# Performance work log

Measured on AMD Instinct MI355X. Metric: run time of the kernel, lower is better.

## Reference

```python
import math
import jax, jax.numpy as jnp
import numpy as np

V_NODES = 100000
E_EDGES = 800000
D_IN = 128
D_OUT = 128
H = 4
F_H = D_OUT // H
LEAK = 0.2


def _xavier(key, shape):
    fan_in, fan_out = shape[0], shape[1]
    lim = math.sqrt(6.0 / (fan_in + fan_out))
    return jax.random.uniform(key, shape, jnp.float32, -lim, lim)


def setup_inputs() -> dict:
    key = jax.random.key(0)
    ks = jax.random.split(key, 10)
    h = jax.random.normal(ks[0], (V_NODES, D_IN), jnp.float32)
    edge_index = jax.random.randint(ks[1], (2, E_EDGES), 0, V_NODES, jnp.int64)
    # omega in {+1, -1, 0}
    edge_weight = jax.random.randint(ks[2], (E_EDGES,), -1, 2).astype(jnp.float32)
    return {
        "h": h,
        "edge_index": edge_index,
        "edge_weight": edge_weight,
        "Wq": _xavier(ks[3], (D_IN, D_OUT)), "bq": jnp.zeros((D_OUT,), jnp.float32),
        "Wk": _xavier(ks[4], (D_IN, D_OUT)), "bk": jnp.zeros((D_OUT,), jnp.float32),
        "Wv": _xavier(ks[5], (D_IN, D_OUT)), "bv": jnp.zeros((D_OUT,), jnp.float32),
        "Wo": _xavier(ks[6], (D_OUT, D_OUT)), "bo": jnp.zeros((D_OUT,), jnp.float32),
        "We": _xavier(ks[7], (1, H)), "be": jnp.zeros((H,), jnp.float32),
        "gamma": jnp.ones((D_OUT,), jnp.float32), "beta": jnp.zeros((D_OUT,), jnp.float32),
    }


def _layer_norm(x, gamma, beta, eps=1e-5):
    mu = jnp.mean(x, axis=-1, keepdims=True)
    var = jnp.var(x, axis=-1, keepdims=True)
    return (x - mu) * jax.lax.rsqrt(var + eps) * gamma + beta


def reference(h, edge_index, edge_weight, Wq, bq, Wk, bk, Wv, bv, Wo, bo, We, be, gamma, beta):
    V = h.shape[0]
    Q = (h @ Wq + bq).reshape(V, H, F_H)
    K = (h @ Wk + bk).reshape(V, H, F_H)
    Vv = (h @ Wv + bv).reshape(V, H, F_H)

    src, tgt = edge_index[0], edge_index[1]
    # edge-aware bias: Proj(omega) with LeakyReLU, [E, H]
    edge_bias = jax.nn.leaky_relu(edge_weight[:, None] * We[0] + be, LEAK)

    # per-edge multi-head scores [E, H]
    attn_raw = jnp.einsum("ehf,ehf->eh", Q[src], K[tgt]) / math.sqrt(F_H)
    attn_raw = attn_raw + edge_bias  # ent_bias = 0 (add_entity_sim=False)
    attn_exp = jnp.exp(attn_raw)

    # degree-based softmax normalization over incoming edges of each target
    deg = jax.ops.segment_sum(attn_exp, tgt, num_segments=V) + 1e-16  # [V, H]
    attn_norm = attn_exp / deg[tgt]  # [E, H]  (dropout rate = 0)

    # weighted message aggregation: alpha * omega * (W_v h_src)
    msg = Vv[src] * attn_norm[:, :, None] * edge_weight[:, None, None]  # [E, H, F_H]
    out = jax.ops.segment_sum(msg, tgt, num_segments=V).reshape(V, H * F_H)

    out = out @ Wo + bo + h  # residual
    out = _layer_norm(out, gamma, beta)
    return jax.nn.leaky_relu(out, LEAK)
```

## Files before the change

kernel.cpp:

```cpp
#include <hip/hip_runtime.h>
#include <math.h>

#define V_NODES 100000
#define E_EDGES 800000
#define HEADS 4
#define FH 32
#define D 128
#define LEAK 0.2f
#define NB 8

__global__ __launch_bounds__(384) void qkv_kernel(
    const float* __restrict__ h,
    const float* __restrict__ Wq, const float* __restrict__ bq,
    const float* __restrict__ Wk, const float* __restrict__ bk,
    const float* __restrict__ Wv, const float* __restrict__ bv,
    float* __restrict__ Q, float* __restrict__ K, float* __restrict__ Vv)
{
    __shared__ float hsh[D][NB];
    const int tid  = threadIdx.x;
    const int base = blockIdx.x * NB;

    for (int idx = tid; idx < NB * D; idx += 384) {
        int n = idx >> 7, k = idx & 127;
        hsh[k][n] = h[(long)(base + n) * D + k];
    }
    __syncthreads();

    const int wsel = tid >> 7;
    const int col  = tid & 127;
    const float* W = (wsel == 0) ? Wq : (wsel == 1) ? Wk : Wv;
    const float* b = (wsel == 0) ? bq : (wsel == 1) ? bk : bv;
    float* O       = (wsel == 0) ? Q  : (wsel == 1) ? K  : Vv;

    float acc[NB];
#pragma unroll
    for (int n = 0; n < NB; n++) acc[n] = 0.f;

    for (int k = 0; k < D; k++) {
        float w = W[k * D + col];
#pragma unroll
        for (int n = 0; n < NB; n++) acc[n] += hsh[k][n] * w;
    }

    float bias = b[col];
#pragma unroll
    for (int n = 0; n < NB; n++) O[(long)(base + n) * D + col] = acc[n] + bias;
}

__global__ __launch_bounds__(256) void score_kernel(
    const int* __restrict__ src, const int* __restrict__ tgt,
    const float* __restrict__ ew,
    const float* __restrict__ Q, const float* __restrict__ K,
    const float* __restrict__ We, const float* __restrict__ be,
    float* __restrict__ attn_exp)
{
    int t = blockIdx.x * 256 + threadIdx.x;
    int e = t >> 4;
    int sub = t & 15;
    if (e >= E_EDGES) return;
    int s = src[e], tg = tgt[e];
    const float4* q4 = (const float4*)(Q + (long)s * D);
    const float4* k4 = (const float4*)(K + (long)tg * D);
    float4 a0 = q4[sub * 2], a1 = q4[sub * 2 + 1];
    float4 b0 = k4[sub * 2], b1 = k4[sub * 2 + 1];
    float p = a0.x * b0.x + a0.y * b0.y + a0.z * b0.z + a0.w * b0.w
            + a1.x * b1.x + a1.y * b1.y + a1.z * b1.z + a1.w * b1.w;
    p += __shfl_xor(p, 1);
    p += __shfl_xor(p, 2);
    if ((sub & 3) == 0) {
        int hh = sub >> 2;
        float w = ew[e];
        float bias = w * We[hh] + be[hh];
        bias = (bias > 0.f) ? bias : LEAK * bias;
        attn_exp[(long)e * 4 + hh] = __expf(p * 0.17677669529663687f + bias);
    }
}

__global__ __launch_bounds__(256) void hist_kernel(
    const int* __restrict__ tgt, int* __restrict__ rs)
{
    int e = blockIdx.x * 256 + threadIdx.x;
    if (e < E_EDGES) atomicAdd(&rs[tgt[e]], 1);
}

__global__ __launch_bounds__(1024) void scan_kernel(int* __restrict__ rs)
{
    __shared__ int part[1024];
    const int tid = threadIdx.x;
    const int CH = (V_NODES + 1023) / 1024;
    int begin = tid * CH;
    int end   = begin + CH; if (end > V_NODES) end = V_NODES;
    if (begin > V_NODES) begin = V_NODES;
    int s = 0;
    for (int i = begin; i < end; i++) s += rs[i];
    part[tid] = s;
    __syncthreads();
    for (int off = 1; off < 1024; off <<= 1) {
        int v = (tid >= off) ? part[tid - off] : 0;
        __syncthreads();
        part[tid] += v;
        __syncthreads();
    }
    int excl = (tid == 0) ? 0 : part[tid - 1];
    for (int i = begin; i < end; i++) {
        int c = rs[i];
        rs[i] = excl;
        excl += c;
    }
}

__global__ __launch_bounds__(256) void scatter_kernel(
    const int* __restrict__ tgt, int* __restrict__ rs, int* __restrict__ csr_e)
{
    int e = blockIdx.x * 256 + threadIdx.x;
    if (e >= E_EDGES) return;
    int pos = atomicAdd(&rs[tgt[e]], 1);
    csr_e[pos] = e;
}

__global__ __launch_bounds__(256) void agg_kernel(
    const int* __restrict__ rs, const int* __restrict__ csr_e,
    const int* __restrict__ src, const float* __restrict__ ew,
    const float* __restrict__ attn_exp,
    const float* __restrict__ Vv, float* __restrict__ out)
{
    int node = blockIdx.x * 4 + (threadIdx.x >> 6);
    if (node >= V_NODES) return;
    int lane = threadIdx.x & 63;
    int hh = lane >> 4;
    int j1 = rs[node];
    int j0 = node ? rs[node - 1] : 0;
    float acc0 = 0.f, acc1 = 0.f, deg = 0.f;
    for (int j = j0; j < j1; j++) {
        int e = csr_e[j];
        float4 att = *((const float4*)(attn_exp + (long)e * 4));
        float atth = (hh == 0) ? att.x : (hh == 1) ? att.y : (hh == 2) ? att.z : att.w;
        deg += atth;
        float w = ew[e];
        if (w != 0.f) {
            float2 v = ((const float2*)(Vv + (long)src[e] * D))[lane];
            float a = atth * w;
            acc0 += a * v.x;
            acc1 += a * v.y;
        }
    }
    float inv = 1.f / (deg + 1e-16f);
    ((float2*)(out + (long)node * D))[lane] = make_float2(acc0 * inv, acc1 * inv);
}

__global__ __launch_bounds__(128) void out_kernel(
    const float* __restrict__ h, const float* __restrict__ Wo,
    const float* __restrict__ bo, const float* __restrict__ gamma,
    const float* __restrict__ beta, float* __restrict__ out)
{
    __shared__ float ash[D][NB];
    __shared__ float red[2][NB][2];
    const int tid  = threadIdx.x;
    const int base = blockIdx.x * NB;
    const int wave = tid >> 6, lane = tid & 63;

#pragma unroll
    for (int n = 0; n < NB; n++) ash[tid][n] = out[(long)(base + n) * D + tid];
    __syncthreads();

    float acc[NB];
#pragma unroll
    for (int n = 0; n < NB; n++) acc[n] = 0.f;
    for (int k = 0; k < D; k++) {
        float w = Wo[k * D + tid];
#pragma unroll
        for (int n = 0; n < NB; n++) acc[n] += ash[k][n] * w;
    }

    float bb = bo[tid];
    float v[NB];
#pragma unroll
    for (int n = 0; n < NB; n++) {
        v[n] = acc[n] + bb + h[(long)(base + n) * D + tid];
        float s = v[n], q = v[n] * v[n];
#pragma unroll
        for (int off = 32; off; off >>= 1) {
            s += __shfl_xor(s, off);
            q += __shfl_xor(q, off);
        }
        if (lane == 0) { red[wave][n][0] = s; red[wave][n][1] = q; }
    }
    __syncthreads();

    float g = gamma[tid], bt = beta[tid];
#pragma unroll
    for (int n = 0; n < NB; n++) {
        float s  = red[0][n][0] + red[1][n][0];
        float q  = red[0][n][1] + red[1][n][1];
        float mu = s * (1.f / 128.f);
        float var = q * (1.f / 128.f) - mu * mu;
        float rstd = rsqrtf(var + 1e-5f);
        float y = (v[n] - mu) * rstd * g + bt;
        out[(long)(base + n) * D + tid] = (y > 0.f) ? y : LEAK * y;
    }
}

extern "C" void kernel_launch(void* const* d_in, const int* in_sizes, int n_in,
                              void* d_out, int out_size, void* d_ws, size_t ws_size,
                              hipStream_t stream)
{
    const float* h     = (const float*)d_in[0];
    const int*   ei    = (const int*)d_in[1];
    const float* ew    = (const float*)d_in[2];
    const float* Wq    = (const float*)d_in[3];
    const float* bq    = (const float*)d_in[4];
    const float* Wk    = (const float*)d_in[5];
    const float* bk    = (const float*)d_in[6];
    const float* Wv    = (const float*)d_in[7];
    const float* bv    = (const float*)d_in[8];
    const float* Wo    = (const float*)d_in[9];
    const float* bo    = (const float*)d_in[10];
    const float* We    = (const float*)d_in[11];
    const float* be    = (const float*)d_in[12];
    const float* gamma = (const float*)d_in[13];
    const float* beta  = (const float*)d_in[14];
    float* out = (float*)d_out;

    float* Q        = (float*)d_ws;
    float* K        = Q  + (size_t)V_NODES * D;
    float* Vv       = K  + (size_t)V_NODES * D;
    float* attn_exp = Vv + (size_t)V_NODES * D;

    int* rs    = (int*)Q;
    int* csr_e = rs + V_NODES;

    const int* srcp = ei;
    const int* tgtp = ei + E_EDGES;

    qkv_kernel<<<V_NODES / NB, 384, 0, stream>>>(h, Wq, bq, Wk, bk, Wv, bv, Q, K, Vv);
    score_kernel<<<(E_EDGES * 16) / 256, 256, 0, stream>>>(srcp, tgtp, ew, Q, K, We, be, attn_exp);

    hipMemsetAsync(rs, 0, V_NODES * sizeof(int), stream);
    hist_kernel<<<(E_EDGES + 255) / 256, 256, 0, stream>>>(tgtp, rs);
    scan_kernel<<<1, 1024, 0, stream>>>(rs);
    scatter_kernel<<<(E_EDGES + 255) / 256, 256, 0, stream>>>(tgtp, rs, csr_e);

    agg_kernel<<<(V_NODES + 3) / 4, 256, 0, stream>>>(rs, csr_e, srcp, ew, attn_exp, Vv, out);
    out_kernel<<<V_NODES / NB, 128, 0, stream>>>(h, Wo, bo, gamma, beta, out);
}
```

Baseline: 911.9 us.

## Compute QKV projection with bf16 MFMA using pre-transposed bf16 weights

Replaces the scalar FP32 QKV projection kernel with a matrix-core version that uses mfma_f32_16x16x32_bf16. A small prep kernel first converts Wq/Wk/Wv to bf16 and transposes them into the workspace. Each block computes 16 rows across all 384 output columns, and the h rows are converted to bf16 in registers. This cuts the ALU cost of the GEMM but lowers the precision of Q, K and V to bf16-rounded inputs, and the strided per-column stores may be poorly coalesced.

Measured after the change: 847.0 us. -7.1%, faster.

```diff
diff --git a/kernel.cpp b/kernel.cpp
--- a/kernel.cpp
+++ b/kernel.cpp
@@ -4,47 +4,83 @@
 #define V_NODES 100000
 #define E_EDGES 800000
 #define HEADS 4
-#define FH 32
 #define D 128
 #define LEAK 0.2f
 #define NB 8
 
-__global__ __launch_bounds__(384) void qkv_kernel(
-    const float* __restrict__ h,
-    const float* __restrict__ Wq, const float* __restrict__ bq,
-    const float* __restrict__ Wk, const float* __restrict__ bk,
-    const float* __restrict__ Wv, const float* __restrict__ bv,
+typedef __attribute__((ext_vector_type(8))) short bf16x8;
+typedef __attribute__((ext_vector_type(4))) float f32x4;
+
+__device__ __forceinline__ unsigned short f2bf(float f) {
+    unsigned u = __float_as_uint(f);
+    u += 0x7FFFu + ((u >> 16) & 1u);
+    return (unsigned short)(u >> 16);
+}
+
+__global__ __launch_bounds__(256) void prep_w(
+    const float* __restrict__ Wq, const float* __restrict__ Wk,
+    const float* __restrict__ Wv,
+    unsigned short* __restrict__ Wt)
+{
+    int idx = blockIdx.x * 256 + threadIdx.x;
+    int c = idx >> 7, k = idx & 127;
+    int m = c >> 7, lc = c & 127;
+    const float* W = (m == 0) ? Wq : (m == 1) ? Wk : Wv;
+    Wt[idx] = f2bf(W[k * D + lc]);
+}
+
+__global__ __launch_bounds__(256) void qkv_mfma(
+    const float* __restrict__ h, const unsigned short* __restrict__ Wt,
+    const float* __restrict__ bq, const float* __restrict__ bk,
+    const float* __restrict__ bv,
     float* __restrict__ Q, float* __restrict__ K, float* __restrict__ Vv)
 {
-    __shared__ float hsh[D][NB];
-    const int tid  = threadIdx.x;
-    const int base = blockIdx.x * NB;
-
-    for (int idx = tid; idx < NB * D; idx += 384) {
-        int n = idx >> 7, k = idx & 127;
-        hsh[k][n] = h[(long)(base + n) * D + k];
-    }
-    __syncthreads();
-
-    const int wsel = tid >> 7;
-    const int col  = tid & 127;
-    const float* W = (wsel == 0) ? Wq : (wsel == 1) ? Wk : Wv;
-    const float* b = (wsel == 0) ? bq : (wsel == 1) ? bk : bv;
-    float* O       = (wsel == 0) ? Q  : (wsel == 1) ? K  : Vv;
-
-    float acc[NB];
-#pragma unroll
-    for (int n = 0; n < NB; n++) acc[n] = 0.f;
-
-    for (int k = 0; k < D; k++) {
-        float w = W[k * D + col];
-#pragma unroll
-        for (int n = 0; n < NB; n++) acc[n] += hsh[k][n] * w;
-    }
-
-    float bias = b[col];
-#pragma unroll
-    for (int n = 0; n < NB; n++) O[(long)(base + n) * D + col] = acc[n] + bias;
+    const int wave = threadIdx.x >> 6, lane = threadIdx.x & 63;
+    const int row0 = blockIdx.x * 16;
+    const int col0 = wave * 96;
+    const int r = lane & 15, g = lane >> 4;
+
+    bf16x8 afrag[4];
+#pragma unroll
+    for (int ks = 0; ks < 4; ks++) {
+        const float* ap = h + (long)(row0 + r) * D + ks * 32 + g * 8;
+        float4 f0 = *(const float4*)ap;
+        float4 f1 = *(const float4*)(ap + 4);
+        bf16x8 a;
+        a[0] = (short)f2bf(f0.x); a[1] = (short)f2bf(f0.y);
+        a[2] = (short)f2bf(f0.z); a[3] = (short)f2bf(f0.w);
+        a[4] = (short)f2bf(f1.x); a[5] = (short)f2bf(f1.y);
+        a[6] = (short)f2bf(f1.z); a[7] = (short)f2bf(f1.w);
+        afrag[ks] = a;
+    }
+
+    f32x4 acc[6];
+#pragma unroll
+    for (int t = 0; t < 6; t++) acc[t] = (f32x4){0.f, 0.f, 0.f, 0.f};
+
+#pragma unroll
+    for (int t = 0; t < 6; t++) {
+        const unsigned short* bp = Wt + (long)(col0 + t * 16 + r) * D;
+#pragma unroll
+        for (int ks = 0; ks < 4; ks++) {
+            bf16x8 bfrag = *(const bf16x8*)(bp + ks * 32 + g * 8);
+            acc[t] = __builtin_amdgcn_mfma_f32_16x16x32_bf16(afrag[ks], bfrag, acc[t], 0, 0, 0);
+        }
+    }
+
+#pragma unroll
+    for (int t = 0; t < 6; t++) {
+        int col = col0 + t * 16 + r;
+        int m = col >> 7, lc = col & 127;
+        const float* bias = (m == 0) ? bq : (m == 1) ? bk : bv;
+        float* O          = (m == 0) ? Q  : (m == 1) ? K  : Vv;
+        float bb = bias[lc];
+#pragma unroll
+        for (int q = 0; q < 4; q++) {
+            int R = row0 + g * 4 + q;
+            O[(long)R * D + lc] = acc[t][q] + bb;
+        }
+    }
 }
 
 __global__ __launch_bounds__(256) void score_kernel(
@@ -89,7 +125,7 @@
     const int tid = threadIdx.x;
     const int CH = (V_NODES + 1023) / 1024;
     int begin = tid * CH;
-    int end   = begin + CH; if (end > V_NODES) end = V_NODES;
+    int end = begin + CH; if (end > V_NODES) end = V_NODES;
     if (begin > V_NODES) begin = V_NODES;
     int s = 0;
     for (int i = begin; i < end; i++) s += rs[i];
@@ -221,25 +257,27 @@
     const float* beta  = (const float*)d_in[14];
     float* out = (float*)d_out;
 
-    float* Q        = (float*)d_ws;
-    float* K        = Q  + (size_t)V_NODES * D;
-    float* Vv       = K  + (size_t)V_NODES * D;
-    float* attn_exp = Vv + (size_t)V_NODES * D;
-
-    int* rs    = (int*)Q;
+    const size_t VD = (size_t)V_NODES * D;
+    float* Qf       = (float*)d_ws;
+    float* Kf       = Qf + VD;
+    float* Vf       = Kf + VD;
+    float* attn_exp = Vf + VD;
+    unsigned short* Wt = (unsigned short*)(attn_exp + (size_t)E_EDGES * 4);
+    int* rs    = (int*)Qf;
     int* csr_e = rs + V_NODES;
 
     const int* srcp = ei;
     const int* tgtp = ei + E_EDGES;
 
-    qkv_kernel<<<V_NODES / NB, 384, 0, stream>>>(h, Wq, bq, Wk, bk, Wv, bv, Q, K, Vv);
-    score_kernel<<<(E_EDGES * 16) / 256, 256, 0, stream>>>(srcp, tgtp, ew, Q, K, We, be, attn_exp);
+    prep_w<<<(384 * 128) / 256, 256, 0, stream>>>(Wq, Wk, Wv, Wt);
+    qkv_mfma<<<V_NODES / 16, 256, 0, stream>>>(h, Wt, bq, bk, bv, Qf, Kf, Vf);
+    score_kernel<<<(E_EDGES * 16) / 256, 256, 0, stream>>>(srcp, tgtp, ew, Qf, Kf, We, be, attn_exp);
 
     hipMemsetAsync(rs, 0, V_NODES * sizeof(int), stream);
     hist_kernel<<<(E_EDGES + 255) / 256, 256, 0, stream>>>(tgtp, rs);
     scan_kernel<<<1, 1024, 0, stream>>>(rs);
     scatter_kernel<<<(E_EDGES + 255) / 256, 256, 0, stream>>>(tgtp, rs, csr_e);
 
-    agg_kernel<<<(V_NODES + 3) / 4, 256, 0, stream>>>(rs, csr_e, srcp, ew, attn_exp, Vv, out);
+    agg_kernel<<<(V_NODES + 3) / 4, 256, 0, stream>>>(rs, csr_e, srcp, ew, attn_exp, Vf, out);
     out_kernel<<<V_NODES / NB, 128, 0, stream>>>(h, Wo, bo, gamma, beta, out);
 }
```
